# Performance work log

Measured on AMD Instinct MI355X. Metric: run time of the kernel, lower is better.

Reference implementation:

```python
import jax, jax.numpy as jnp
import numpy as np

B, N = 64, 4096

def setup_inputs() -> dict:
    key = jax.random.key(0)
    k1, k2, k3, k4, k5, k6 = jax.random.split(key, 6)
    return {
        "V_mag": jax.random.uniform(k1, (B, N), dtype=jnp.float32, minval=0.9, maxval=1.1),
        "V_ang": 0.3 * jax.random.normal(k2, (B, N), dtype=jnp.float32),
        "P_in": jax.random.normal(k3, (B, N), dtype=jnp.float32),
        "Q_in": jax.random.normal(k4, (B, N), dtype=jnp.float32),
        "G_bus": jax.random.normal(k5, (N, N), dtype=jnp.float32) / np.sqrt(N),
        "B_bus": jax.random.normal(k6, (N, N), dtype=jnp.float32) / np.sqrt(N),
    }

def reference(V_mag, V_ang, P_in, Q_in, G_bus, B_bus):
    # P_i = V_i sum_j V_j (G_ij cos(ti-tj) + B_ij sin(ti-tj))
    # Q_i = V_i sum_j V_j (G_ij sin(ti-tj) - B_ij cos(ti-tj))
    # Angle-addition rewrite (exact): with c_j = V_j cos(t_j), s_j = V_j sin(t_j):
    #   sum_j G_ij V_j cos(ti-tj) = cos(ti)*(G c)_i + sin(ti)*(G s)_i, etc.
    cos_t = jnp.cos(V_ang)  # [B, N]
    sin_t = jnp.sin(V_ang)
    c = V_mag * cos_t       # V_j cos(t_j)
    s = V_mag * sin_t       # V_j sin(t_j)
    Gc = jnp.einsum('ij,bj->bi', G_bus, c)
    Gs = jnp.einsum('ij,bj->bi', G_bus, s)
    Bc = jnp.einsum('ij,bj->bi', B_bus, c)
    Bs = jnp.einsum('ij,bj->bi', B_bus, s)
    # sum_j V_j (G cos + B sin) = cos_ti*(Gc+Bs) + sin_ti*(Gs-Bc)
    P_calc = V_mag * (cos_t * (Gc + Bs) + sin_t * (Gs - Bc))
    # sum_j V_j (G sin - B cos) = sin_ti*(Gc+Bs) - cos_ti*(Gs-Bc)
    Q_calc = V_mag * (sin_t * (Gc + Bs) - cos_t * (Gs - Bc))
    res_P = P_calc - P_in
    res_Q = Q_calc - Q_in
    return (res_P, res_Q)
```

## Files before the change

### kernel.cpp

```cpp
#include <hip/hip_runtime.h>
#include <stdint.h>

#define N_DIM 4096
#define B_DIM 64

typedef __bf16 bf16x8 __attribute__((ext_vector_type(8)));
typedef float floatx4 __attribute__((ext_vector_type(4)));

union FragU { uint4 u; bf16x8 h; };

__device__ __forceinline__ unsigned short f2bf_rne(float f) {
    unsigned int u = __float_as_uint(f);
    u += 0x7fffu + ((u >> 16) & 1u);
    return (unsigned short)(u >> 16);
}

__global__ __launch_bounds__(256) void pf_prep(
        const float* __restrict__ Vmag, const float* __restrict__ Vang,
        unsigned short* __restrict__ c_pk, unsigned short* __restrict__ s_pk) {
    int idx = blockIdx.x * 256 + threadIdx.x;
    int b = idx >> 12;
    int j = idx & 4095;
    float sv, cv;
    sincosf(Vang[idx], &sv, &cv);
    float v = Vmag[idx];
    int p = (((j >> 3) << 6) + b) * 8 + (j & 7);
    c_pk[p] = f2bf_rne(v * cv);
    s_pk[p] = f2bf_rne(v * sv);
}

__global__ __launch_bounds__(1024) void pf_gemm(
        const float* __restrict__ G, const float* __restrict__ Bm,
        const unsigned short* __restrict__ c_pk, const unsigned short* __restrict__ s_pk,
        const float* __restrict__ Vmag, const float* __restrict__ Vang,
        const float* __restrict__ P_in, const float* __restrict__ Q_in,
        float* __restrict__ out) {
    __shared__ __align__(16) float red[2 * 4 * 16 * 66];
    const int tid = threadIdx.x;
    const int wave = tid >> 6;
    const int lane = tid & 63;
    const int n = lane & 15;
    const int quad = lane >> 4;
    const int ch = wave & 1;
    const int w8 = wave >> 1;
    const int i0 = blockIdx.x << 4;

    const float* gp = G  + (size_t)(i0 + n) * N_DIM + w8 * 512 + quad * 8;
    const float* bp = Bm + (size_t)(i0 + n) * N_DIM + w8 * 512 + quad * 8;
    const unsigned short* cp = c_pk + ((size_t)((w8 * 64 + quad) * 64) + ch * 32 + n) * 8;
    const unsigned short* sp = s_pk + ((size_t)((w8 * 64 + quad) * 64) + ch * 32 + n) * 8;

    floatx4 accX[2], accY[2];
    #pragma unroll
    for (int t16 = 0; t16 < 2; ++t16) {
        accX[t16] = (floatx4){0.f, 0.f, 0.f, 0.f};
        accY[t16] = (floatx4){0.f, 0.f, 0.f, 0.f};
    }

    float4 g0 = *(const float4*)(gp);
    float4 g1 = *(const float4*)(gp + 4);
    float4 h0 = *(const float4*)(bp);
    float4 h1 = *(const float4*)(bp + 4);
    uint4 cu[2], su[2];
    cu[0] = *(const uint4*)(cp);
    cu[1] = *(const uint4*)(cp + 128);
    su[0] = *(const uint4*)(sp);
    su[1] = *(const uint4*)(sp + 128);

    #pragma unroll
    for (int t = 0; t < 16; ++t) {
        bf16x8 ag, ah;
        ag[0] = (__bf16)g0.x; ag[1] = (__bf16)g0.y; ag[2] = (__bf16)g0.z; ag[3] = (__bf16)g0.w;
        ag[4] = (__bf16)g1.x; ag[5] = (__bf16)g1.y; ag[6] = (__bf16)g1.z; ag[7] = (__bf16)g1.w;
        ah[0] = (__bf16)h0.x; ah[1] = (__bf16)h0.y; ah[2] = (__bf16)h0.z; ah[3] = (__bf16)h0.w;
        ah[4] = (__bf16)h1.x; ah[5] = (__bf16)h1.y; ah[6] = (__bf16)h1.z; ah[7] = (__bf16)h1.w;

        uint4 ncu[2], nsu[2];
        if (t < 15) {
            const float* g2 = gp + (t + 1) * 32;
            const float* b2 = bp + (t + 1) * 32;
            g0 = *(const float4*)(g2);
            g1 = *(const float4*)(g2 + 4);
            h0 = *(const float4*)(b2);
            h1 = *(const float4*)(b2 + 4);
            const unsigned short* cpt = cp + (size_t)(t + 1) * 2048;
            const unsigned short* spt = sp + (size_t)(t + 1) * 2048;
            ncu[0] = *(const uint4*)(cpt);
            ncu[1] = *(const uint4*)(cpt + 128);
            nsu[0] = *(const uint4*)(spt);
            nsu[1] = *(const uint4*)(spt + 128);
        }

        #pragma unroll
        for (int t16 = 0; t16 < 2; ++t16) {
            FragU cf, nf;
            cf.u = cu[t16];
            nf.u.x = cu[t16].x ^ 0x80008000u;
            nf.u.y = cu[t16].y ^ 0x80008000u;
            nf.u.z = cu[t16].z ^ 0x80008000u;
            nf.u.w = cu[t16].w ^ 0x80008000u;
            accX[t16] = __builtin_amdgcn_mfma_f32_16x16x32_bf16(ag, cf.h, accX[t16], 0, 0, 0);
            accY[t16] = __builtin_amdgcn_mfma_f32_16x16x32_bf16(ah, nf.h, accY[t16], 0, 0, 0);
        }
        #pragma unroll
        for (int t16 = 0; t16 < 2; ++t16) {
            FragU sf;
            sf.u = su[t16];
            accX[t16] = __builtin_amdgcn_mfma_f32_16x16x32_bf16(ah, sf.h, accX[t16], 0, 0, 0);
            accY[t16] = __builtin_amdgcn_mfma_f32_16x16x32_bf16(ag, sf.h, accY[t16], 0, 0, 0);
        }

        if (t < 15) {
            cu[0] = ncu[0]; cu[1] = ncu[1];
            su[0] = nsu[0]; su[1] = nsu[1];
        }
    }

    #define RED(x, wp, m, b) red[(((x) * 4 + (wp)) * 16 + (m)) * 66 + (b)]
    if (w8 >= 4) {
        #pragma unroll
        for (int t16 = 0; t16 < 2; ++t16)
            #pragma unroll
            for (int r = 0; r < 4; ++r) {
                RED(0, w8 - 4, (quad << 2) + r, ch * 32 + (t16 << 4) + n) = accX[t16][r];
                RED(1, w8 - 4, (quad << 2) + r, ch * 32 + (t16 << 4) + n) = accY[t16][r];
            }
    }
    __syncthreads();
    if (w8 < 4) {
        #pragma unroll
        for (int t16 = 0; t16 < 2; ++t16)
            #pragma unroll
            for (int r = 0; r < 4; ++r) {
                RED(0, w8, (quad << 2) + r, ch * 32 + (t16 << 4) + n) += accX[t16][r];
                RED(1, w8, (quad << 2) + r, ch * 32 + (t16 << 4) + n) += accY[t16][r];
            }
    }
    __syncthreads();

    {
        int bb = tid >> 4;
        int m = tid & 15;
        float X = 0.f, Y = 0.f;
        #pragma unroll
        for (int w = 0; w < 4; ++w) {
            X += RED(0, w, m, bb);
            Y += RED(1, w, m, bb);
        }
        size_t off = (size_t)bb * N_DIM + i0 + m;
        float sv, cv;
        sincosf(Vang[off], &sv, &cv);
        float v = Vmag[off];
        float c = v * cv;
        float s = v * sv;
        out[off] = c * X + s * Y - P_in[off];
        out[(size_t)B_DIM * N_DIM + off] = s * X - c * Y - Q_in[off];
    }
}

extern "C" void kernel_launch(void* const* d_in, const int* in_sizes, int n_in,
                              void* d_out, int out_size, void* d_ws, size_t ws_size,
                              hipStream_t stream) {
    const float* Vmag = (const float*)d_in[0];
    const float* Vang = (const float*)d_in[1];
    const float* P_in = (const float*)d_in[2];
    const float* Q_in = (const float*)d_in[3];
    const float* G    = (const float*)d_in[4];
    const float* Bm   = (const float*)d_in[5];
    float* out = (float*)d_out;

    char* ws = (char*)d_ws;
    unsigned short* c_pk = (unsigned short*)(ws);
    unsigned short* s_pk = (unsigned short*)(ws + (512u << 10));

    hipLaunchKernelGGL(pf_prep, dim3((B_DIM * N_DIM) / 256), dim3(256), 0, stream,
                       Vmag, Vang, c_pk, s_pk);
    hipLaunchKernelGGL(pf_gemm, dim3(N_DIM / 16), dim3(1024), 0, stream,
                       G, Bm, c_pk, s_pk, Vmag, Vang, P_in, Q_in, out);
}
```

Baseline: 175.8 us.

## Deepen global-load prefetch to two stages with inline asm and explicit vmcnt waits

Replaces the one-step register prefetch of G/B rows and packed c/s fragments with a three-slot ring for G/B (prefetch distance two) and double buffering for c/s. The loads are issued as inline-asm global_load_dwordx4 with SGPR base and 32-bit VGPR offsets, and the code waits with explicit s_waitcnt vmcnt counts behind sched barriers. The aim is to keep more HBM loads in flight per wave so the streaming GEMV-like kernel hides memory latency better. In exchange it raises register pressure at 1024 threads per block, and the hand-counted vmcnt values must match the load issue order exactly or the kernel reads stale data.

```diff
diff --git a/kernel.cpp b/kernel.cpp
--- a/kernel.cpp
+++ b/kernel.cpp
@@ -29,6 +29,19 @@
     s_pk[p] = f2bf_rne(v * sv);
 }
 
+__device__ __forceinline__ float4 aload_f4(const float* base, uint32_t boff) {
+    float4 d;
+    asm volatile("global_load_dwordx4 %0, %1, %2"
+                 : "=v"(d) : "v"(boff), "s"(base));
+    return d;
+}
+__device__ __forceinline__ uint4 aload_u4(const unsigned short* base, uint32_t boff) {
+    uint4 d;
+    asm volatile("global_load_dwordx4 %0, %1, %2"
+                 : "=v"(d) : "v"(boff), "s"(base));
+    return d;
+}
+
 __global__ __launch_bounds__(1024) void pf_gemm(
         const float* __restrict__ G, const float* __restrict__ Bm,
         const unsigned short* __restrict__ c_pk, const unsigned short* __restrict__ s_pk,
@@ -45,10 +58,8 @@
     const int w8 = wave >> 1;
     const int i0 = blockIdx.x << 4;
 
-    const float* gp = G  + (size_t)(i0 + n) * N_DIM + w8 * 512 + quad * 8;
-    const float* bp = Bm + (size_t)(i0 + n) * N_DIM + w8 * 512 + quad * 8;
-    const unsigned short* cp = c_pk + ((size_t)((w8 * 64 + quad) * 64) + ch * 32 + n) * 8;
-    const unsigned short* sp = s_pk + ((size_t)((w8 * 64 + quad) * 64) + ch * 32 + n) * 8;
+    const uint32_t goff  = ((uint32_t)(i0 + n) * N_DIM + w8 * 512 + quad * 8) * 4u;
+    const uint32_t csoff = ((uint32_t)((w8 * 64 + quad) * 64) + ch * 32 + n) * 16u;
 
     floatx4 accX[2], accY[2];
     #pragma unroll
@@ -57,62 +68,69 @@
         accY[t16] = (floatx4){0.f, 0.f, 0.f, 0.f};
     }
 
-    float4 g0 = *(const float4*)(gp);
-    float4 g1 = *(const float4*)(gp + 4);
-    float4 h0 = *(const float4*)(bp);
-    float4 h1 = *(const float4*)(bp + 4);
-    uint4 cu[2], su[2];
-    cu[0] = *(const uint4*)(cp);
-    cu[1] = *(const uint4*)(cp + 128);
-    su[0] = *(const uint4*)(sp);
-    su[1] = *(const uint4*)(sp + 128);
+    float4 gA[3][2], hA[3][2];
+    uint4  cu[2][2], su[2][2];
+
+    gA[0][0] = aload_f4(G,  goff);
+    gA[0][1] = aload_f4(G,  goff + 16);
+    hA[0][0] = aload_f4(Bm, goff);
+    hA[0][1] = aload_f4(Bm, goff + 16);
+    gA[1][0] = aload_f4(G,  goff + 128);
+    gA[1][1] = aload_f4(G,  goff + 144);
+    hA[1][0] = aload_f4(Bm, goff + 128);
+    hA[1][1] = aload_f4(Bm, goff + 144);
+    cu[0][0] = aload_u4(c_pk, csoff);
+    cu[0][1] = aload_u4(c_pk, csoff + 256);
+    su[0][0] = aload_u4(s_pk, csoff);
+    su[0][1] = aload_u4(s_pk, csoff + 256);
 
     #pragma unroll
     for (int t = 0; t < 16; ++t) {
+        if (t + 2 < 16) {
+            const uint32_t og = goff + (uint32_t)(t + 2) * 128u;
+            gA[(t + 2) % 3][0] = aload_f4(G,  og);
+            gA[(t + 2) % 3][1] = aload_f4(G,  og + 16);
+            hA[(t + 2) % 3][0] = aload_f4(Bm, og);
+            hA[(t + 2) % 3][1] = aload_f4(Bm, og + 16);
+        }
+        if (t + 1 < 16) {
+            const uint32_t oc = csoff + (uint32_t)(t + 1) * 4096u;
+            cu[(t + 1) & 1][0] = aload_u4(c_pk, oc);
+            cu[(t + 1) & 1][1] = aload_u4(c_pk, oc + 256);
+            su[(t + 1) & 1][0] = aload_u4(s_pk, oc);
+            su[(t + 1) & 1][1] = aload_u4(s_pk, oc + 256);
+        }
+        __builtin_amdgcn_sched_barrier(0);
+        if (t < 14)       asm volatile("s_waitcnt vmcnt(8)");
+        else if (t == 14) asm volatile("s_waitcnt vmcnt(4)");
+        else              asm volatile("s_waitcnt vmcnt(0)");
+        __builtin_amdgcn_sched_barrier(0);
+
+        const float4 g0 = gA[t % 3][0], g1 = gA[t % 3][1];
+        const float4 h0 = hA[t % 3][0], h1 = hA[t % 3][1];
         bf16x8 ag, ah;
         ag[0] = (__bf16)g0.x; ag[1] = (__bf16)g0.y; ag[2] = (__bf16)g0.z; ag[3] = (__bf16)g0.w;
         ag[4] = (__bf16)g1.x; ag[5] = (__bf16)g1.y; ag[6] = (__bf16)g1.z; ag[7] = (__bf16)g1.w;
         ah[0] = (__bf16)h0.x; ah[1] = (__bf16)h0.y; ah[2] = (__bf16)h0.z; ah[3] = (__bf16)h0.w;
         ah[4] = (__bf16)h1.x; ah[5] = (__bf16)h1.y; ah[6] = (__bf16)h1.z; ah[7] = (__bf16)h1.w;
 
-        uint4 ncu[2], nsu[2];
-        if (t < 15) {
-            const float* g2 = gp + (t + 1) * 32;
-            const float* b2 = bp + (t + 1) * 32;
-            g0 = *(const float4*)(g2);
-            g1 = *(const float4*)(g2 + 4);
-            h0 = *(const float4*)(b2);
-            h1 = *(const float4*)(b2 + 4);
-            const unsigned short* cpt = cp + (size_t)(t + 1) * 2048;
-            const unsigned short* spt = sp + (size_t)(t + 1) * 2048;
-            ncu[0] = *(const uint4*)(cpt);
-            ncu[1] = *(const uint4*)(cpt + 128);
-            nsu[0] = *(const uint4*)(spt);
-            nsu[1] = *(const uint4*)(spt + 128);
-        }
-
         #pragma unroll
         for (int t16 = 0; t16 < 2; ++t16) {
             FragU cf, nf;
-            cf.u = cu[t16];
-            nf.u.x = cu[t16].x ^ 0x80008000u;
-            nf.u.y = cu[t16].y ^ 0x80008000u;
-            nf.u.z = cu[t16].z ^ 0x80008000u;
-            nf.u.w = cu[t16].w ^ 0x80008000u;
+            cf.u = cu[t & 1][t16];
+            nf.u.x = cf.u.x ^ 0x80008000u;
+            nf.u.y = cf.u.y ^ 0x80008000u;
+            nf.u.z = cf.u.z ^ 0x80008000u;
+            nf.u.w = cf.u.w ^ 0x80008000u;
             accX[t16] = __builtin_amdgcn_mfma_f32_16x16x32_bf16(ag, cf.h, accX[t16], 0, 0, 0);
             accY[t16] = __builtin_amdgcn_mfma_f32_16x16x32_bf16(ah, nf.h, accY[t16], 0, 0, 0);
         }
         #pragma unroll
         for (int t16 = 0; t16 < 2; ++t16) {
             FragU sf;
-            sf.u = su[t16];
+            sf.u = su[t & 1][t16];
             accX[t16] = __builtin_amdgcn_mfma_f32_16x16x32_bf16(ah, sf.h, accX[t16], 0, 0, 0);
             accY[t16] = __builtin_amdgcn_mfma_f32_16x16x32_bf16(ag, sf.h, accY[t16], 0, 0, 0);
-        }
-
-        if (t < 15) {
-            cu[0] = ncu[0]; cu[1] = ncu[1];
-            su[0] = nsu[0]; su[1] = nsu[1];
         }
     }
 
```

Result: no change. 176.7 us (+0.5%).
